# Kernel optimization log

Measured on AMD Instinct MI355X. Metric: run time of the kernel, lower is better.

The kernel has to match this reference:

```python
import jax, jax.numpy as jnp
import numpy as np

NUM_C = 1000
DIM_S = 128
SIZE_M = 64
B = 64
L = 512


def setup_inputs() -> dict:
    key = jax.random.key(0)
    ks = jax.random.split(key, 16)
    d = DIM_S
    inp = {
        "q": jax.random.randint(ks[0], (B, L), 0, NUM_C),
        "r": jax.random.randint(ks[1], (B, L), 0, 2),
        # embeddings
        "Ek": jax.random.normal(ks[2], (NUM_C, d), jnp.float32),
        "Ev": jax.random.normal(ks[3], (2 * NUM_C, d), jnp.float32),
        # memory key / initial value memory (kaiming-normal-ish)
        "Mk": jax.random.normal(ks[4], (SIZE_M, d), jnp.float32) * np.sqrt(2.0 / d),
        "Mv0": jax.random.normal(ks[5], (SIZE_M, d), jnp.float32) * np.sqrt(2.0 / d),
        # erase / add layers (d -> d)
        "We": jax.random.normal(ks[6], (d, d), jnp.float32) / np.sqrt(d),
        "be": jnp.zeros((d,), jnp.float32),
        "Wa": jax.random.normal(ks[7], (d, d), jnp.float32) / np.sqrt(d),
        "ba": jnp.zeros((d,), jnp.float32),
        # f layer (2d -> d)
        "Wf": jax.random.normal(ks[8], (2 * d, d), jnp.float32) / np.sqrt(2 * d),
        "bf": jnp.zeros((d,), jnp.float32),
        # p layer (d -> 1)
        "Wp": jax.random.normal(ks[9], (d, 1), jnp.float32) / np.sqrt(d),
        "bp": jnp.zeros((1,), jnp.float32),
    }
    return inp


def reference(q, r, Ek, Ev, Mk, Mv0, We, be, Wa, ba, Wf, bf, Wp, bp):
    # q, r: [B, L] int
    x = q + NUM_C * r
    k = Ek[q]            # [B, L, D]  (k_original; no extra features when use_ed=use_mp=0)
    v = Ev[x]            # [B, L, D]

    # correlation weights over memory slots
    w = jax.nn.softmax(jnp.einsum("bld,md->blm", k, Mk), axis=-1)  # [B, L, M]

    e = jax.nn.sigmoid(v @ We + be)  # [B, L, D] erase
    a = jnp.tanh(v @ Wa + ba)        # [B, L, D] add

    def step(Mvt, inputs):
        wt, et, at = inputs            # [B,M], [B,D], [B,D]
        # read from memory BEFORE the update (matches Mv[:, :-1] in torch)
        read = jnp.einsum("bm,bmd->bd", wt, Mvt)
        Mvt_new = Mvt * (1.0 - wt[:, :, None] * et[:, None, :]) + wt[:, :, None] * at[:, None, :]
        return Mvt_new, read

    Mv_init = jnp.broadcast_to(Mv0[None], (q.shape[0], SIZE_M, DIM_S))
    xs = (jnp.swapaxes(w, 0, 1), jnp.swapaxes(e, 0, 1), jnp.swapaxes(a, 0, 1))
    _, reads = jax.lax.scan(step, Mv_init, xs)      # reads: [L, B, D]
    read_content = jnp.swapaxes(reads, 0, 1)        # [B, L, D]

    f = jnp.tanh(jnp.concatenate([read_content, k], axis=-1) @ Wf + bf)  # [B, L, D]
    # dropout in eval mode -> identity
    p = jax.nn.sigmoid(f @ Wp + bp)[..., 0]         # [B, L]
    return p
```

## Files before the change

### kernel.cpp

```cpp
#include <hip/hip_runtime.h>
#include <hip/hip_bf16.h>

#define NUM_C 1000
#define DIM   128
#define MM    64
#define BB    64
#define LL    512
#define NROWS (BB * LL)

typedef unsigned short u16;
typedef unsigned int   u32;
typedef short bfrag __attribute__((ext_vector_type(8)));
typedef float f32x4 __attribute__((ext_vector_type(4)));

__device__ __forceinline__ float sigmoidf_fast(float x) { return 1.f / (1.f + __expf(-x)); }
__device__ __forceinline__ float tanhf_fast(float x) { return 1.f - 2.f / (__expf(2.f * x) + 1.f); }

__device__ __forceinline__ u16 f2bf(float x) {
    u32 u = __float_as_uint(x);
    return (u16)((u + 0x7FFFu + ((u >> 16) & 1u)) >> 16);
}
__device__ __forceinline__ float bf2f(u16 h) { return __uint_as_float(((u32)h) << 16); }

__device__ __forceinline__ float quad_swap1(float x) {
    return __int_as_float(__builtin_amdgcn_mov_dpp(__float_as_int(x), 0xB1, 0xF, 0xF, true));
}
__device__ __forceinline__ float quad_swap2(float x) {
    return __int_as_float(__builtin_amdgcn_mov_dpp(__float_as_int(x), 0x4E, 0xF, 0xF, true));
}

__device__ __forceinline__ void ld16(const void* g, void* l) {
    __builtin_amdgcn_global_load_lds(
        (const __attribute__((address_space(1))) unsigned int*)g,
        (__attribute__((address_space(3))) unsigned int*)l, 16, 0, 0);
}

__global__ __launch_bounds__(256) void kP(const float* __restrict__ We,
                                          const float* __restrict__ Wa,
                                          const float* __restrict__ Wf,
                                          const float* __restrict__ Mk,
                                          u16* weT_hi, u16* weT_lo,
                                          u16* waT_hi, u16* waT_lo,
                                          u16* wfT_hi, u16* wfT_lo,
                                          u16* mkT_hi, u16* mkT_lo) {
    int idx = blockIdx.x * 256 + threadIdx.x;
    if (idx < 128 * 128) {
        int n = idx >> 7, k = idx & 127;
        float we = We[k * DIM + n];
        u16 h = f2bf(we);
        weT_hi[idx] = h; weT_lo[idx] = f2bf(we - bf2f(h));
        float wa = Wa[k * DIM + n];
        u16 h2 = f2bf(wa);
        waT_hi[idx] = h2; waT_lo[idx] = f2bf(wa - bf2f(h2));
    }
    if (idx < 64 * 128) {
        float mk = Mk[idx];
        u16 h = f2bf(mk);
        mkT_hi[idx] = h; mkT_lo[idx] = f2bf(mk - bf2f(h));
    }
    {
        int n = idx >> 8, k = idx & 255;
        float wf = Wf[k * DIM + n];
        u16 h = f2bf(wf);
        wfT_hi[idx] = h; wfT_lo[idx] = f2bf(wf - bf2f(h));
    }
}

__device__ __forceinline__ void split8(const float* src, bfrag& h, bfrag& l) {
    float4 f0 = *reinterpret_cast<const float4*>(src);
    float4 f1 = *reinterpret_cast<const float4*>(src + 4);
    float xs[8] = {f0.x, f0.y, f0.z, f0.w, f1.x, f1.y, f1.z, f1.w};
    #pragma unroll
    for (int j = 0; j < 8; ++j) {
        u16 hb = f2bf(xs[j]);
        h[j] = (short)hb;
        l[j] = (short)f2bf(xs[j] - bf2f(hb));
    }
}

__global__ __launch_bounds__(256) void kA(const int* __restrict__ q,
                                          const float* __restrict__ Ek,
                                          const u16* __restrict__ mkT_hi,
                                          const u16* __restrict__ mkT_lo,
                                          float* __restrict__ w_out) {
    __shared__ __align__(16) u16 khi[4][16][136];
    __shared__ __align__(16) u16 klo[4][16][136];
    __shared__ float slab[4][64];
    const int tid = threadIdx.x;
    const int base = blockIdx.x * 64;

    {
        const int row_l = tid >> 2;
        const int rts = row_l >> 4, ms = row_l & 15;
        const int d0 = (tid & 3) * 32;
        const float* src = Ek + (size_t)q[base + row_l] * DIM + d0;
        #pragma unroll
        for (int c8 = 0; c8 < 4; ++c8) {
            bfrag h, l;
            split8(src + c8 * 8, h, l);
            *reinterpret_cast<bfrag*>(&khi[rts][ms][d0 + c8 * 8]) = h;
            *reinterpret_cast<bfrag*>(&klo[rts][ms][d0 + c8 * 8]) = l;
        }
    }
    __syncthreads();

    const int lane = tid & 63;
    const int wv = tid >> 6;
    const int nloc = lane & 15;
    const int quad = lane >> 4;
    const int n = wv * 16 + nloc;

    bfrag Bh[4], Bl[4];
    #pragma unroll
    for (int kc = 0; kc < 4; ++kc) {
        const int ko = kc * 32 + quad * 8;
        Bh[kc] = *reinterpret_cast<const bfrag*>(mkT_hi + n * DIM + ko);
        Bl[kc] = *reinterpret_cast<const bfrag*>(mkT_lo + n * DIM + ko);
    }

    f32x4 acc[4];
    #pragma unroll
    for (int t = 0; t < 4; ++t) acc[t] = 0.f;

    #pragma unroll
    for (int rt = 0; rt < 4; ++rt) {
        #pragma unroll
        for (int kc = 0; kc < 4; ++kc) {
            const int ko = kc * 32 + quad * 8;
            bfrag Ah = *reinterpret_cast<const bfrag*>(&khi[rt][nloc][ko]);
            bfrag Al = *reinterpret_cast<const bfrag*>(&klo[rt][nloc][ko]);
            acc[rt] = __builtin_amdgcn_mfma_f32_16x16x32_bf16(Ah, Bh[kc], acc[rt], 0, 0, 0);
            acc[rt] = __builtin_amdgcn_mfma_f32_16x16x32_bf16(Ah, Bl[kc], acc[rt], 0, 0, 0);
            acc[rt] = __builtin_amdgcn_mfma_f32_16x16x32_bf16(Al, Bh[kc], acc[rt], 0, 0, 0);
        }
    }

    float ex[4][4];
    #pragma unroll
    for (int rt = 0; rt < 4; ++rt) {
        #pragma unroll
        for (int rg = 0; rg < 4; ++rg) {
            float e = __expf(acc[rt][rg]);
            ex[rt][rg] = e;
            float s = e;
            s += __shfl_xor(s, 1);
            s += __shfl_xor(s, 2);
            s += __shfl_xor(s, 4);
            s += __shfl_xor(s, 8);
            if (nloc == 0) slab[wv][rt * 16 + quad * 4 + rg] = s;
        }
    }
    __syncthreads();

    #pragma unroll
    for (int rt = 0; rt < 4; ++rt) {
        #pragma unroll
        for (int rg = 0; rg < 4; ++rg) {
            const int row = rt * 16 + quad * 4 + rg;
            float tot = slab[0][row] + slab[1][row] + slab[2][row] + slab[3][row];
            w_out[(size_t)(base + row) * MM + n] = ex[rt][rg] / tot;
        }
    }
}

__global__ __launch_bounds__(256) void kB(const int* __restrict__ q,
                                          const int* __restrict__ r,
                                          const float* __restrict__ Ev,
                                          const u16* __restrict__ weT_hi, const u16* __restrict__ weT_lo,
                                          const u16* __restrict__ waT_hi, const u16* __restrict__ waT_lo,
                                          const float* __restrict__ be, const float* __restrict__ ba,
                                          float2* __restrict__ ea_out) {
    __shared__ __align__(16) u16 vhi[4][16][136];
    __shared__ __align__(16) u16 vlo[4][16][136];
    const int tid = threadIdx.x;
    const int base = blockIdx.x * 64;

    {
        const int row_l = tid >> 2;
        const int rts = row_l >> 4, ms = row_l & 15;
        const int d0 = (tid & 3) * 32;
        const int row = base + row_l;
        const int x = q[row] + NUM_C * r[row];
        const float* src = Ev + (size_t)x * DIM + d0;
        #pragma unroll
        for (int c8 = 0; c8 < 4; ++c8) {
            bfrag h, l;
            split8(src + c8 * 8, h, l);
            *reinterpret_cast<bfrag*>(&vhi[rts][ms][d0 + c8 * 8]) = h;
            *reinterpret_cast<bfrag*>(&vlo[rts][ms][d0 + c8 * 8]) = l;
        }
    }
    __syncthreads();

    const int lane = tid & 63;
    const int wv = tid >> 6;
    const int nloc = lane & 15;
    const int quad = lane >> 4;

    #pragma unroll
    for (int dt = 0; dt < 2; ++dt) {
        const int n = (wv * 2 + dt) * 16 + nloc;
        bfrag Beh[4], Bel[4], Bah[4], Bal[4];
        #pragma unroll
        for (int kc = 0; kc < 4; ++kc) {
            const int ko = kc * 32 + quad * 8;
            Beh[kc] = *reinterpret_cast<const bfrag*>(weT_hi + n * DIM + ko);
            Bel[kc] = *reinterpret_cast<const bfrag*>(weT_lo + n * DIM + ko);
            Bah[kc] = *reinterpret_cast<const bfrag*>(waT_hi + n * DIM + ko);
            Bal[kc] = *reinterpret_cast<const bfrag*>(waT_lo + n * DIM + ko);
        }
        f32x4 acc_e[4], acc_a[4];
        #pragma unroll
        for (int t = 0; t < 4; ++t) { acc_e[t] = 0.f; acc_a[t] = 0.f; }

        #pragma unroll
        for (int rt = 0; rt < 4; ++rt) {
            #pragma unroll
            for (int kc = 0; kc < 4; ++kc) {
                const int ko = kc * 32 + quad * 8;
                bfrag Ah = *reinterpret_cast<const bfrag*>(&vhi[rt][nloc][ko]);
                bfrag Al = *reinterpret_cast<const bfrag*>(&vlo[rt][nloc][ko]);
                acc_e[rt] = __builtin_amdgcn_mfma_f32_16x16x32_bf16(Ah, Beh[kc], acc_e[rt], 0, 0, 0);
                acc_a[rt] = __builtin_amdgcn_mfma_f32_16x16x32_bf16(Ah, Bah[kc], acc_a[rt], 0, 0, 0);
                acc_e[rt] = __builtin_amdgcn_mfma_f32_16x16x32_bf16(Ah, Bel[kc], acc_e[rt], 0, 0, 0);
                acc_a[rt] = __builtin_amdgcn_mfma_f32_16x16x32_bf16(Ah, Bal[kc], acc_a[rt], 0, 0, 0);
                acc_e[rt] = __builtin_amdgcn_mfma_f32_16x16x32_bf16(Al, Beh[kc], acc_e[rt], 0, 0, 0);
                acc_a[rt] = __builtin_amdgcn_mfma_f32_16x16x32_bf16(Al, Bah[kc], acc_a[rt], 0, 0, 0);
            }
        }
        const float bev = be[n], bav = ba[n];
        #pragma unroll
        for (int rt = 0; rt < 4; ++rt) {
            #pragma unroll
            for (int rg = 0; rg < 4; ++rg) {
                const int row = base + rt * 16 + quad * 4 + rg;
                float2 ea;
                ea.x = sigmoidf_fast(acc_e[rt][rg] + bev);
                ea.y = tanhf_fast(acc_a[rt][rg] + bav);
                ea_out[(size_t)row * DIM + n] = ea;
            }
        }
    }
}

__device__ __forceinline__ void scan32(const float* wb, const float2* eab,
                                       int m0, int dl, int p, int t0,
                                       float (&Mv)[8], float* rp2) {
    #pragma unroll
    for (int u = 0; u < 32; ++u) {
        float4 w0 = *reinterpret_cast<const float4*>(wb + u * 64 + m0);
        float4 w1 = *reinterpret_cast<const float4*>(wb + u * 64 + m0 + 4);
        float2 ea = eab[u * 32 + dl];
        float wv[8] = {w0.x, w0.y, w0.z, w0.w, w1.x, w1.y, w1.z, w1.w};
        float e_c = ea.x, a_c = ea.y;
        float p0 = 0.f, p1 = 0.f;
        #pragma unroll
        for (int j = 0; j < 4; ++j) {
            float old = Mv[j];
            p0 = fmaf(wv[j], old, p0);
            Mv[j] = fmaf(wv[j], fmaf(-old, e_c, a_c), old);
        }
        #pragma unroll
        for (int j = 4; j < 8; ++j) {
            float old = Mv[j];
            p1 = fmaf(wv[j], old, p1);
            Mv[j] = fmaf(wv[j], fmaf(-old, e_c, a_c), old);
        }
        float part = p0 + p1;
        part += quad_swap1(part);
        part += quad_swap2(part);
        if ((p & 3) == 0)
            rp2[(size_t)(t0 + u) * (2 * DIM)] = part;
    }
}

__global__ __launch_bounds__(256) void kC(const float* __restrict__ Mv0,
                                          const float* __restrict__ w_in,
                                          const float2* __restrict__ ea_in,
                                          float* __restrict__ rd2) {
    __shared__ __align__(16) float  wlds[2][32][64];
    __shared__ __align__(16) float2 ealds[2][32][32];
    const int tid = threadIdx.x;
    const int lane = tid & 63;
    const int wvid = tid >> 6;
    const int p = tid & 7;
    const int dl = tid >> 3;
    const int ds = blockIdx.x, b = blockIdx.y;
    const int d = ds * 32 + dl;
    const int m0 = p * 8;

    const char* wsrc  = (const char*)(w_in + (size_t)b * LL * MM);
    const char* easrc = (const char*)(ea_in + (size_t)b * LL * DIM + ds * 32);
    float* rp2 = rd2 + (size_t)b * LL * (2 * DIM) + (size_t)d * 2 + (p >> 2);

    auto dma = [&](int c, int bufi) {
        const char* wt = wsrc + (size_t)c * 8192;
        char* wl = (char*)&wlds[bufi][0][0];
        char* el = (char*)&ealds[bufi][0][0];
        #pragma unroll
        for (int i = 0; i < 2; ++i) {
            const int off = wvid * 2048 + i * 1024 + lane * 16;
            ld16(wt + off, wl + off);
            const int tl = off >> 8, wi = off & 255;
            ld16(easrc + (size_t)(c * 32 + tl) * (DIM * 8) + wi, el + off);
        }
    };

    dma(0, 0);

    float Mv[8];
    #pragma unroll
    for (int j = 0; j < 8; ++j)
        Mv[j] = Mv0[(m0 + j) * DIM + d];

    __builtin_amdgcn_s_waitcnt(0x0F70);
    __syncthreads();

    int buf = 0;
    for (int c = 0; c < LL / 32; ++c) {
        if (c + 1 < LL / 32) dma(c + 1, buf ^ 1);
        scan32(&wlds[buf][0][0], &ealds[buf][0][0], m0, dl, p, c * 32, Mv, rp2);
        if (c + 1 < LL / 32) {
            __builtin_amdgcn_s_waitcnt(0x8F70);
            __syncthreads();
            buf ^= 1;
        }
    }
}

__global__ __launch_bounds__(256) void kD(const int* __restrict__ q,
                                          const float* __restrict__ Ek,
                                          const u16* __restrict__ wfT_hi, const u16* __restrict__ wfT_lo,
                                          const float* __restrict__ bfv,
                                          const float* __restrict__ Wp, const float* __restrict__ bp,
                                          const float* __restrict__ rd2,
                                          float* __restrict__ out) {
    __shared__ __align__(16) u16 xhi[4][16][264];
    __shared__ __align__(16) u16 xlo[4][16][264];
    __shared__ float sred[64][4];
    const int tid = threadIdx.x;
    const int base = blockIdx.x * 64;
    const int row_l = tid >> 2;
    const int rts = row_l >> 4, ms = row_l & 15;
    const int d0 = (tid & 3) * 32;
    const int row = base + row_l;

    {
        const float2* src2 = reinterpret_cast<const float2*>(rd2 + (size_t)row * (2 * DIM)) + d0;
        #pragma unroll
        for (int c8 = 0; c8 < 4; ++c8) {
            float xs[8];
            #pragma unroll
            for (int j = 0; j < 8; ++j) {
                float2 v = src2[c8 * 8 + j];
                xs[j] = v.x + v.y;
            }
            bfrag h, l;
            #pragma unroll
            for (int j = 0; j < 8; ++j) {
                u16 hb = f2bf(xs[j]);
                h[j] = (short)hb;
                l[j] = (short)f2bf(xs[j] - bf2f(hb));
            }
            *reinterpret_cast<bfrag*>(&xhi[rts][ms][d0 + c8 * 8]) = h;
            *reinterpret_cast<bfrag*>(&xlo[rts][ms][d0 + c8 * 8]) = l;
        }
    }
    {
        const float* src = Ek + (size_t)q[row] * DIM + d0;
        #pragma unroll
        for (int c8 = 0; c8 < 4; ++c8) {
            bfrag h, l;
            split8(src + c8 * 8, h, l);
            *reinterpret_cast<bfrag*>(&xhi[rts][ms][128 + d0 + c8 * 8]) = h;
            *reinterpret_cast<bfrag*>(&xlo[rts][ms][128 + d0 + c8 * 8]) = l;
        }
    }
    __syncthreads();

    const int lane = tid & 63;
    const int wv = tid >> 6;
    const int nloc = lane & 15;
    const int quad = lane >> 4;
    float* fbuf = reinterpret_cast<float*>(&xhi[0][0][0]);

    f32x4 acc[2][4];
    #pragma unroll
    for (int dt = 0; dt < 2; ++dt)
        #pragma unroll
        for (int t = 0; t < 4; ++t) acc[dt][t] = 0.f;

    #pragma unroll
    for (int dt = 0; dt < 2; ++dt) {
        const int n = (wv * 2 + dt) * 16 + nloc;
        bfrag Bh[8], Bl[8];
        #pragma unroll
        for (int kc = 0; kc < 8; ++kc) {
            const int ko = kc * 32 + quad * 8;
            Bh[kc] = *reinterpret_cast<const bfrag*>(wfT_hi + n * 256 + ko);
            Bl[kc] = *reinterpret_cast<const bfrag*>(wfT_lo + n * 256 + ko);
        }
        #pragma unroll
        for (int rt = 0; rt < 4; ++rt) {
            #pragma unroll
            for (int kc = 0; kc < 8; ++kc) {
                const int ko = kc * 32 + quad * 8;
                bfrag Ah = *reinterpret_cast<const bfrag*>(&xhi[rt][nloc][ko]);
                bfrag Al = *reinterpret_cast<const bfrag*>(&xlo[rt][nloc][ko]);
                acc[dt][rt] = __builtin_amdgcn_mfma_f32_16x16x32_bf16(Ah, Bh[kc], acc[dt][rt], 0, 0, 0);
                acc[dt][rt] = __builtin_amdgcn_mfma_f32_16x16x32_bf16(Ah, Bl[kc], acc[dt][rt], 0, 0, 0);
                acc[dt][rt] = __builtin_amdgcn_mfma_f32_16x16x32_bf16(Al, Bh[kc], acc[dt][rt], 0, 0, 0);
            }
        }
    }
    __syncthreads();

    #pragma unroll
    for (int dt = 0; dt < 2; ++dt) {
        const int n = (wv * 2 + dt) * 16 + nloc;
        const float bfn = bfv[n], wpn = Wp[n];
        #pragma unroll
        for (int rt = 0; rt < 4; ++rt)
            #pragma unroll
            for (int rg = 0; rg < 4; ++rg)
                fbuf[(rt * 16 + quad * 4 + rg) * 132 + n] = tanhf_fast(acc[dt][rt][rg] + bfn) * wpn;
    }
    __syncthreads();

    {
        float s = 0.f;
        const int c = tid & 3;
        #pragma unroll
        for (int k = 0; k < 32; ++k) s += fbuf[row_l * 132 + c * 32 + k];
        sred[row_l][c] = s;
    }
    __syncthreads();
    if (tid < 64)
        out[base + tid] = sigmoidf_fast(sred[tid][0] + sred[tid][1] + sred[tid][2] + sred[tid][3] + bp[0]);
}

extern "C" void kernel_launch(void* const* d_in, const int* in_sizes, int n_in,
                              void* d_out, int out_size, void* d_ws, size_t ws_size,
                              hipStream_t stream) {
    const int*   q   = (const int*)d_in[0];
    const int*   r   = (const int*)d_in[1];
    const float* Ek  = (const float*)d_in[2];
    const float* Ev  = (const float*)d_in[3];
    const float* Mk  = (const float*)d_in[4];
    const float* Mv0 = (const float*)d_in[5];
    const float* We  = (const float*)d_in[6];
    const float* be  = (const float*)d_in[7];
    const float* Wa  = (const float*)d_in[8];
    const float* ba  = (const float*)d_in[9];
    const float* Wf  = (const float*)d_in[10];
    const float* bfv = (const float*)d_in[11];
    const float* Wp  = (const float*)d_in[12];
    const float* bp  = (const float*)d_in[13];
    float* out = (float*)d_out;

    float*  ws     = (float*)d_ws;
    float*  w_buf  = ws;
    float2* ea_buf = (float2*)(w_buf + (size_t)NROWS * MM);
    float*  rd2    = (float*)(ea_buf + (size_t)NROWS * DIM);

    size_t prep_off = (ws_size - (size_t)294912) & ~(size_t)255;
    u16* weT_hi = (u16*)((char*)d_ws + prep_off);
    u16* weT_lo = weT_hi + 16384;
    u16* waT_hi = weT_lo + 16384;
    u16* waT_lo = waT_hi + 16384;
    u16* wfT_hi = waT_lo + 16384;
    u16* wfT_lo = wfT_hi + 32768;
    u16* mkT_hi = wfT_lo + 32768;
    u16* mkT_lo = mkT_hi + 8192;

    kP<<<dim3(128), 256, 0, stream>>>(We, Wa, Wf, Mk, weT_hi, weT_lo, waT_hi, waT_lo,
                                      wfT_hi, wfT_lo, mkT_hi, mkT_lo);
    kA<<<dim3(NROWS / 64), 256, 0, stream>>>(q, Ek, mkT_hi, mkT_lo, w_buf);
    kB<<<dim3(NROWS / 64), 256, 0, stream>>>(q, r, Ev, weT_hi, weT_lo, waT_hi, waT_lo,
                                             be, ba, ea_buf);
    kC<<<dim3(4, BB), 256, 0, stream>>>(Mv0, w_buf, ea_buf, rd2);
    kD<<<dim3(NROWS / 64), 256, 0, stream>>>(q, Ek, wfT_hi, wfT_lo, bfv, Wp, bp, rd2, out);
}
```

Before: 192.5 us.

## Merge embedding-projection kernels and split memory scan across twice as many blocks

The separate softmax-weight kernel and erase/add kernel are merged into one launch, with a block-index branch selecting which job each block does. The recurrent memory-scan kernel now uses 8 feature slices per batch row instead of 4, so each thread updates 4 memory slots instead of 8. That doubles the number of scan blocks and shortens each thread's per-step dependency work. In exchange, the read buffer holds four partial sums per feature instead of two. This doubles its footprint and the traffic the final kernel must read and reduce, and it depends on the workspace being large enough.

```diff
diff --git a/kernel.cpp b/kernel.cpp
--- a/kernel.cpp
+++ b/kernel.cpp
@@ -78,166 +78,155 @@
     }
 }
 
-__global__ __launch_bounds__(256) void kA(const int* __restrict__ q,
-                                          const float* __restrict__ Ek,
-                                          const u16* __restrict__ mkT_hi,
-                                          const u16* __restrict__ mkT_lo,
-                                          float* __restrict__ w_out) {
-    __shared__ __align__(16) u16 khi[4][16][136];
-    __shared__ __align__(16) u16 klo[4][16][136];
+__global__ __launch_bounds__(256) void kAB(const int* __restrict__ q,
+                                           const int* __restrict__ r,
+                                           const float* __restrict__ Ek,
+                                           const float* __restrict__ Ev,
+                                           const u16* __restrict__ mkT_hi, const u16* __restrict__ mkT_lo,
+                                           const u16* __restrict__ weT_hi, const u16* __restrict__ weT_lo,
+                                           const u16* __restrict__ waT_hi, const u16* __restrict__ waT_lo,
+                                           const float* __restrict__ be, const float* __restrict__ ba,
+                                           float* __restrict__ w_out,
+                                           float2* __restrict__ ea_out) {
+    __shared__ __align__(16) u16 shi[4][16][136];
+    __shared__ __align__(16) u16 slo[4][16][136];
     __shared__ float slab[4][64];
     const int tid = threadIdx.x;
-    const int base = blockIdx.x * 64;
-
-    {
-        const int row_l = tid >> 2;
-        const int rts = row_l >> 4, ms = row_l & 15;
-        const int d0 = (tid & 3) * 32;
-        const float* src = Ek + (size_t)q[base + row_l] * DIM + d0;
-        #pragma unroll
-        for (int c8 = 0; c8 < 4; ++c8) {
-            bfrag h, l;
-            split8(src + c8 * 8, h, l);
-            *reinterpret_cast<bfrag*>(&khi[rts][ms][d0 + c8 * 8]) = h;
-            *reinterpret_cast<bfrag*>(&klo[rts][ms][d0 + c8 * 8]) = l;
-        }
-    }
-    __syncthreads();
-
     const int lane = tid & 63;
     const int wv = tid >> 6;
     const int nloc = lane & 15;
     const int quad = lane >> 4;
-    const int n = wv * 16 + nloc;
-
-    bfrag Bh[4], Bl[4];
-    #pragma unroll
-    for (int kc = 0; kc < 4; ++kc) {
-        const int ko = kc * 32 + quad * 8;
-        Bh[kc] = *reinterpret_cast<const bfrag*>(mkT_hi + n * DIM + ko);
-        Bl[kc] = *reinterpret_cast<const bfrag*>(mkT_lo + n * DIM + ko);
-    }
-
-    f32x4 acc[4];
-    #pragma unroll
-    for (int t = 0; t < 4; ++t) acc[t] = 0.f;
-
-    #pragma unroll
-    for (int rt = 0; rt < 4; ++rt) {
+
+    if (blockIdx.x < 512) {
+        const int base = blockIdx.x * 64;
+        {
+            const int row_l = tid >> 2;
+            const int rts = row_l >> 4, ms = row_l & 15;
+            const int d0 = (tid & 3) * 32;
+            const float* src = Ek + (size_t)q[base + row_l] * DIM + d0;
+            #pragma unroll
+            for (int c8 = 0; c8 < 4; ++c8) {
+                bfrag h, l;
+                split8(src + c8 * 8, h, l);
+                *reinterpret_cast<bfrag*>(&shi[rts][ms][d0 + c8 * 8]) = h;
+                *reinterpret_cast<bfrag*>(&slo[rts][ms][d0 + c8 * 8]) = l;
+            }
+        }
+        __syncthreads();
+
+        const int n = wv * 16 + nloc;
+        bfrag Bh[4], Bl[4];
         #pragma unroll
         for (int kc = 0; kc < 4; ++kc) {
             const int ko = kc * 32 + quad * 8;
-            bfrag Ah = *reinterpret_cast<const bfrag*>(&khi[rt][nloc][ko]);
-            bfrag Al = *reinterpret_cast<const bfrag*>(&klo[rt][nloc][ko]);
-            acc[rt] = __builtin_amdgcn_mfma_f32_16x16x32_bf16(Ah, Bh[kc], acc[rt], 0, 0, 0);
-            acc[rt] = __builtin_amdgcn_mfma_f32_16x16x32_bf16(Ah, Bl[kc], acc[rt], 0, 0, 0);
-            acc[rt] = __builtin_amdgcn_mfma_f32_16x16x32_bf16(Al, Bh[kc], acc[rt], 0, 0, 0);
-        }
-    }
-
-    float ex[4][4];
-    #pragma unroll
-    for (int rt = 0; rt < 4; ++rt) {
-        #pragma unroll
-        for (int rg = 0; rg < 4; ++rg) {
-            float e = __expf(acc[rt][rg]);
-            ex[rt][rg] = e;
-            float s = e;
-            s += __shfl_xor(s, 1);
-            s += __shfl_xor(s, 2);
-            s += __shfl_xor(s, 4);
-            s += __shfl_xor(s, 8);
-            if (nloc == 0) slab[wv][rt * 16 + quad * 4 + rg] = s;
-        }
-    }
-    __syncthreads();
-
-    #pragma unroll
-    for (int rt = 0; rt < 4; ++rt) {
-        #pragma unroll
-        for (int rg = 0; rg < 4; ++rg) {
-            const int row = rt * 16 + quad * 4 + rg;
-            float tot = slab[0][row] + slab[1][row] + slab[2][row] + slab[3][row];
-            w_out[(size_t)(base + row) * MM + n] = ex[rt][rg] / tot;
-        }
-    }
-}
-
-__global__ __launch_bounds__(256) void kB(const int* __restrict__ q,
-                                          const int* __restrict__ r,
-                                          const float* __restrict__ Ev,
-                                          const u16* __restrict__ weT_hi, const u16* __restrict__ weT_lo,
-                                          const u16* __restrict__ waT_hi, const u16* __restrict__ waT_lo,
-                                          const float* __restrict__ be, const float* __restrict__ ba,
-                                          float2* __restrict__ ea_out) {
-    __shared__ __align__(16) u16 vhi[4][16][136];
-    __shared__ __align__(16) u16 vlo[4][16][136];
-    const int tid = threadIdx.x;
-    const int base = blockIdx.x * 64;
-
-    {
-        const int row_l = tid >> 2;
-        const int rts = row_l >> 4, ms = row_l & 15;
-        const int d0 = (tid & 3) * 32;
-        const int row = base + row_l;
-        const int x = q[row] + NUM_C * r[row];
-        const float* src = Ev + (size_t)x * DIM + d0;
-        #pragma unroll
-        for (int c8 = 0; c8 < 4; ++c8) {
-            bfrag h, l;
-            split8(src + c8 * 8, h, l);
-            *reinterpret_cast<bfrag*>(&vhi[rts][ms][d0 + c8 * 8]) = h;
-            *reinterpret_cast<bfrag*>(&vlo[rts][ms][d0 + c8 * 8]) = l;
-        }
-    }
-    __syncthreads();
-
-    const int lane = tid & 63;
-    const int wv = tid >> 6;
-    const int nloc = lane & 15;
-    const int quad = lane >> 4;
-
-    #pragma unroll
-    for (int dt = 0; dt < 2; ++dt) {
-        const int n = (wv * 2 + dt) * 16 + nloc;
-        bfrag Beh[4], Bel[4], Bah[4], Bal[4];
-        #pragma unroll
-        for (int kc = 0; kc < 4; ++kc) {
-            const int ko = kc * 32 + quad * 8;
-            Beh[kc] = *reinterpret_cast<const bfrag*>(weT_hi + n * DIM + ko);
-            Bel[kc] = *reinterpret_cast<const bfrag*>(weT_lo + n * DIM + ko);
-            Bah[kc] = *reinterpret_cast<const bfrag*>(waT_hi + n * DIM + ko);
-            Bal[kc] = *reinterpret_cast<const bfrag*>(waT_lo + n * DIM + ko);
-        }
-        f32x4 acc_e[4], acc_a[4];
-        #pragma unroll
-        for (int t = 0; t < 4; ++t) { acc_e[t] = 0.f; acc_a[t] = 0.f; }
+            Bh[kc] = *reinterpret_cast<const bfrag*>(mkT_hi + n * DIM + ko);
+            Bl[kc] = *reinterpret_cast<const bfrag*>(mkT_lo + n * DIM + ko);
+        }
+
+        f32x4 acc[4];
+        #pragma unroll
+        for (int t = 0; t < 4; ++t) acc[t] = 0.f;
 
         #pragma unroll
         for (int rt = 0; rt < 4; ++rt) {
             #pragma unroll
             for (int kc = 0; kc < 4; ++kc) {
                 const int ko = kc * 32 + quad * 8;
-                bfrag Ah = *reinterpret_cast<const bfrag*>(&vhi[rt][nloc][ko]);
-                bfrag Al = *reinterpret_cast<const bfrag*>(&vlo[rt][nloc][ko]);
-                acc_e[rt] = __builtin_amdgcn_mfma_f32_16x16x32_bf16(Ah, Beh[kc], acc_e[rt], 0, 0, 0);
-                acc_a[rt] = __builtin_amdgcn_mfma_f32_16x16x32_bf16(Ah, Bah[kc], acc_a[rt], 0, 0, 0);
-                acc_e[rt] = __builtin_amdgcn_mfma_f32_16x16x32_bf16(Ah, Bel[kc], acc_e[rt], 0, 0, 0);
-                acc_a[rt] = __builtin_amdgcn_mfma_f32_16x16x32_bf16(Ah, Bal[kc], acc_a[rt], 0, 0, 0);
-                acc_e[rt] = __builtin_amdgcn_mfma_f32_16x16x32_bf16(Al, Beh[kc], acc_e[rt], 0, 0, 0);
-                acc_a[rt] = __builtin_amdgcn_mfma_f32_16x16x32_bf16(Al, Bah[kc], acc_a[rt], 0, 0, 0);
-            }
-        }
-        const float bev = be[n], bav = ba[n];
+                bfrag Ah = *reinterpret_cast<const bfrag*>(&shi[rt][nloc][ko]);
+                bfrag Al = *reinterpret_cast<const bfrag*>(&slo[rt][nloc][ko]);
+                acc[rt] = __builtin_amdgcn_mfma_f32_16x16x32_bf16(Ah, Bh[kc], acc[rt], 0, 0, 0);
+                acc[rt] = __builtin_amdgcn_mfma_f32_16x16x32_bf16(Ah, Bl[kc], acc[rt], 0, 0, 0);
+                acc[rt] = __builtin_amdgcn_mfma_f32_16x16x32_bf16(Al, Bh[kc], acc[rt], 0, 0, 0);
+            }
+        }
+
+        float ex[4][4];
         #pragma unroll
         for (int rt = 0; rt < 4; ++rt) {
             #pragma unroll
             for (int rg = 0; rg < 4; ++rg) {
-                const int row = base + rt * 16 + quad * 4 + rg;
-                float2 ea;
-                ea.x = sigmoidf_fast(acc_e[rt][rg] + bev);
-                ea.y = tanhf_fast(acc_a[rt][rg] + bav);
-                ea_out[(size_t)row * DIM + n] = ea;
+                float e = __expf(acc[rt][rg]);
+                ex[rt][rg] = e;
+                float s = e;
+                s += __shfl_xor(s, 1);
+                s += __shfl_xor(s, 2);
+                s += __shfl_xor(s, 4);
+                s += __shfl_xor(s, 8);
+                if (nloc == 0) slab[wv][rt * 16 + quad * 4 + rg] = s;
+            }
+        }
+        __syncthreads();
+
+        #pragma unroll
+        for (int rt = 0; rt < 4; ++rt) {
+            #pragma unroll
+            for (int rg = 0; rg < 4; ++rg) {
+                const int row = rt * 16 + quad * 4 + rg;
+                float tot = slab[0][row] + slab[1][row] + slab[2][row] + slab[3][row];
+                w_out[(size_t)(base + row) * MM + n] = ex[rt][rg] / tot;
+            }
+        }
+    } else {
+        const int base = (blockIdx.x - 512) * 64;
+        {
+            const int row_l = tid >> 2;
+            const int rts = row_l >> 4, ms = row_l & 15;
+            const int d0 = (tid & 3) * 32;
+            const int row = base + row_l;
+            const int x = q[row] + NUM_C * r[row];
+            const float* src = Ev + (size_t)x * DIM + d0;
+            #pragma unroll
+            for (int c8 = 0; c8 < 4; ++c8) {
+                bfrag h, l;
+                split8(src + c8 * 8, h, l);
+                *reinterpret_cast<bfrag*>(&shi[rts][ms][d0 + c8 * 8]) = h;
+                *reinterpret_cast<bfrag*>(&slo[rts][ms][d0 + c8 * 8]) = l;
+            }
+        }
+        __syncthreads();
+
+        #pragma unroll
+        for (int dt = 0; dt < 2; ++dt) {
+            const int n = (wv * 2 + dt) * 16 + nloc;
+            bfrag Beh[4], Bel[4], Bah[4], Bal[4];
+            #pragma unroll
+            for (int kc = 0; kc < 4; ++kc) {
+                const int ko = kc * 32 + quad * 8;
+                Beh[kc] = *reinterpret_cast<const bfrag*>(weT_hi + n * DIM + ko);
+                Bel[kc] = *reinterpret_cast<const bfrag*>(weT_lo + n * DIM + ko);
+                Bah[kc] = *reinterpret_cast<const bfrag*>(waT_hi + n * DIM + ko);
+                Bal[kc] = *reinterpret_cast<const bfrag*>(waT_lo + n * DIM + ko);
+            }
+            f32x4 acc_e[4], acc_a[4];
+            #pragma unroll
+            for (int t = 0; t < 4; ++t) { acc_e[t] = 0.f; acc_a[t] = 0.f; }
+
+            #pragma unroll
+            for (int rt = 0; rt < 4; ++rt) {
+                #pragma unroll
+                for (int kc = 0; kc < 4; ++kc) {
+                    const int ko = kc * 32 + quad * 8;
+                    bfrag Ah = *reinterpret_cast<const bfrag*>(&shi[rt][nloc][ko]);
+                    bfrag Al = *reinterpret_cast<const bfrag*>(&slo[rt][nloc][ko]);
+                    acc_e[rt] = __builtin_amdgcn_mfma_f32_16x16x32_bf16(Ah, Beh[kc], acc_e[rt], 0, 0, 0);
+                    acc_a[rt] = __builtin_amdgcn_mfma_f32_16x16x32_bf16(Ah, Bah[kc], acc_a[rt], 0, 0, 0);
+                    acc_e[rt] = __builtin_amdgcn_mfma_f32_16x16x32_bf16(Ah, Bel[kc], acc_e[rt], 0, 0, 0);
+                    acc_a[rt] = __builtin_amdgcn_mfma_f32_16x16x32_bf16(Ah, Bal[kc], acc_a[rt], 0, 0, 0);
+                    acc_e[rt] = __builtin_amdgcn_mfma_f32_16x16x32_bf16(Al, Beh[kc], acc_e[rt], 0, 0, 0);
+                    acc_a[rt] = __builtin_amdgcn_mfma_f32_16x16x32_bf16(Al, Bah[kc], acc_a[rt], 0, 0, 0);
+                }
+            }
+            const float bev = be[n], bav = ba[n];
+            #pragma unroll
+            for (int rt = 0; rt < 4; ++rt) {
+                #pragma unroll
+                for (int rg = 0; rg < 4; ++rg) {
+                    const int row = base + rt * 16 + quad * 4 + rg;
+                    float2 ea;
+                    ea.x = sigmoidf_fast(acc_e[rt][rg] + bev);
+                    ea.y = tanhf_fast(acc_a[rt][rg] + bav);
+                    ea_out[(size_t)row * DIM + n] = ea;
+                }
             }
         }
     }
@@ -245,53 +234,45 @@
 
 __device__ __forceinline__ void scan32(const float* wb, const float2* eab,
                                        int m0, int dl, int p, int t0,
-                                       float (&Mv)[8], float* rp2) {
+                                       float (&Mv)[4], float* rp4) {
     #pragma unroll
     for (int u = 0; u < 32; ++u) {
-        float4 w0 = *reinterpret_cast<const float4*>(wb + u * 64 + m0);
-        float4 w1 = *reinterpret_cast<const float4*>(wb + u * 64 + m0 + 4);
-        float2 ea = eab[u * 32 + dl];
-        float wv[8] = {w0.x, w0.y, w0.z, w0.w, w1.x, w1.y, w1.z, w1.w};
+        float4 w4 = *reinterpret_cast<const float4*>(wb + u * 64 + m0);
+        float2 ea = eab[u * 16 + dl];
+        float wv[4] = {w4.x, w4.y, w4.z, w4.w};
         float e_c = ea.x, a_c = ea.y;
-        float p0 = 0.f, p1 = 0.f;
+        float part = 0.f;
         #pragma unroll
         for (int j = 0; j < 4; ++j) {
             float old = Mv[j];
-            p0 = fmaf(wv[j], old, p0);
+            part = fmaf(wv[j], old, part);
             Mv[j] = fmaf(wv[j], fmaf(-old, e_c, a_c), old);
         }
-        #pragma unroll
-        for (int j = 4; j < 8; ++j) {
-            float old = Mv[j];
-            p1 = fmaf(wv[j], old, p1);
-            Mv[j] = fmaf(wv[j], fmaf(-old, e_c, a_c), old);
-        }
-        float part = p0 + p1;
         part += quad_swap1(part);
         part += quad_swap2(part);
         if ((p & 3) == 0)
-            rp2[(size_t)(t0 + u) * (2 * DIM)] = part;
+            rp4[(size_t)(t0 + u) * (DIM * 4)] = part;
     }
 }
 
 __global__ __launch_bounds__(256) void kC(const float* __restrict__ Mv0,
                                           const float* __restrict__ w_in,
                                           const float2* __restrict__ ea_in,
-                                          float* __restrict__ rd2) {
+                                          float* __restrict__ rd4) {
     __shared__ __align__(16) float  wlds[2][32][64];
-    __shared__ __align__(16) float2 ealds[2][32][32];
+    __shared__ __align__(16) float2 ealds[2][32][16];
     const int tid = threadIdx.x;
     const int lane = tid & 63;
     const int wvid = tid >> 6;
-    const int p = tid & 7;
-    const int dl = tid >> 3;
+    const int p = tid & 15;
+    const int dl = tid >> 4;
     const int ds = blockIdx.x, b = blockIdx.y;
-    const int d = ds * 32 + dl;
-    const int m0 = p * 8;
+    const int d = ds * 16 + dl;
+    const int m0 = p * 4;
 
     const char* wsrc  = (const char*)(w_in + (size_t)b * LL * MM);
-    const char* easrc = (const char*)(ea_in + (size_t)b * LL * DIM + ds * 32);
-    float* rp2 = rd2 + (size_t)b * LL * (2 * DIM) + (size_t)d * 2 + (p >> 2);
+    const char* easrc = (const char*)(ea_in + (size_t)b * LL * DIM + ds * 16);
+    float* rp4 = rd4 + (size_t)b * LL * (DIM * 4) + (size_t)d * 4 + (p >> 2);
 
     auto dma = [&](int c, int bufi) {
         const char* wt = wsrc + (size_t)c * 8192;
@@ -301,16 +282,17 @@
         for (int i = 0; i < 2; ++i) {
             const int off = wvid * 2048 + i * 1024 + lane * 16;
             ld16(wt + off, wl + off);
-            const int tl = off >> 8, wi = off & 255;
-            ld16(easrc + (size_t)(c * 32 + tl) * (DIM * 8) + wi, el + off);
-        }
+        }
+        const int off2 = wvid * 1024 + lane * 16;
+        const int tl = off2 >> 7, wi = off2 & 127;
+        ld16(easrc + (size_t)(c * 32 + tl) * (DIM * 8) + wi, el + off2);
     };
 
     dma(0, 0);
 
-    float Mv[8];
-    #pragma unroll
-    for (int j = 0; j < 8; ++j)
+    float Mv[4];
+    #pragma unroll
+    for (int j = 0; j < 4; ++j)
         Mv[j] = Mv0[(m0 + j) * DIM + d];
 
     __builtin_amdgcn_s_waitcnt(0x0F70);
@@ -319,7 +301,7 @@
     int buf = 0;
     for (int c = 0; c < LL / 32; ++c) {
         if (c + 1 < LL / 32) dma(c + 1, buf ^ 1);
-        scan32(&wlds[buf][0][0], &ealds[buf][0][0], m0, dl, p, c * 32, Mv, rp2);
+        scan32(&wlds[buf][0][0], &ealds[buf][0][0], m0, dl, p, c * 32, Mv, rp4);
         if (c + 1 < LL / 32) {
             __builtin_amdgcn_s_waitcnt(0x8F70);
             __syncthreads();
@@ -333,7 +315,7 @@
                                           const u16* __restrict__ wfT_hi, const u16* __restrict__ wfT_lo,
                                           const float* __restrict__ bfv,
                                           const float* __restrict__ Wp, const float* __restrict__ bp,
-                                          const float* __restrict__ rd2,
+                                          const float* __restrict__ rd4,
                                           float* __restrict__ out) {
     __shared__ __align__(16) u16 xhi[4][16][264];
     __shared__ __align__(16) u16 xlo[4][16][264];
@@ -346,14 +328,14 @@
     const int row = base + row_l;
 
     {
-        const float2* src2 = reinterpret_cast<const float2*>(rd2 + (size_t)row * (2 * DIM)) + d0;
+        const float4* src4 = reinterpret_cast<const float4*>(rd4 + (size_t)row * (DIM * 4)) + d0;
         #pragma unroll
         for (int c8 = 0; c8 < 4; ++c8) {
             float xs[8];
             #pragma unroll
             for (int j = 0; j < 8; ++j) {
-                float2 v = src2[c8 * 8 + j];
-                xs[j] = v.x + v.y;
+                float4 v = src4[c8 * 8 + j];
+                xs[j] = (v.x + v.y) + (v.z + v.w);
             }
             bfrag h, l;
             #pragma unroll
@@ -461,7 +443,7 @@
     float*  ws     = (float*)d_ws;
     float*  w_buf  = ws;
     float2* ea_buf = (float2*)(w_buf + (size_t)NROWS * MM);
-    float*  rd2    = (float*)(ea_buf + (size_t)NROWS * DIM);
+    float*  rd4    = (float*)(ea_buf + (size_t)NROWS * DIM);
 
     size_t prep_off = (ws_size - (size_t)294912) & ~(size_t)255;
     u16* weT_hi = (u16*)((char*)d_ws + prep_off);
@@ -475,9 +457,9 @@
 
     kP<<<dim3(128), 256, 0, stream>>>(We, Wa, Wf, Mk, weT_hi, weT_lo, waT_hi, waT_lo,
                                       wfT_hi, wfT_lo, mkT_hi, mkT_lo);
-    kA<<<dim3(NROWS / 64), 256, 0, stream>>>(q, Ek, mkT_hi, mkT_lo, w_buf);
-    kB<<<dim3(NROWS / 64), 256, 0, stream>>>(q, r, Ev, weT_hi, weT_lo, waT_hi, waT_lo,
-                                             be, ba, ea_buf);
-    kC<<<dim3(4, BB), 256, 0, stream>>>(Mv0, w_buf, ea_buf, rd2);
-    kD<<<dim3(NROWS / 64), 256, 0, stream>>>(q, Ek, wfT_hi, wfT_lo, bfv, Wp, bp, rd2, out);
-}
+    kAB<<<dim3(1024), 256, 0, stream>>>(q, r, Ek, Ev, mkT_hi, mkT_lo,
+                                        weT_hi, weT_lo, waT_hi, waT_lo,
+                                        be, ba, w_buf, ea_buf);
+    kC<<<dim3(8, BB), 256, 0, stream>>>(Mv0, w_buf, ea_buf, rd4);
+    kD<<<dim3(NROWS / 64), 256, 0, stream>>>(q, Ek, wfT_hi, wfT_lo, bfv, Wp, bp, rd4, out);
+}
```

Result: faster. 182.7 us (-5.1%).
